# Optimization experiments

Hardware: AMD Instinct MI355X
Metric: run time of the kernel (lower is better)

The kernel has to match this reference:

```python
import jax, jax.numpy as jnp
import numpy as np

N_HEAD = 12
NEG_INF = -1e30


def setup_inputs() -> dict:
    key = jax.random.key(0)
    ks = jax.random.split(key, 12)
    bs, q_len, c_len, d = 2, 2048, 2048, 768
    s = 1.0 / np.sqrt(d)
    return {
        "query": jax.random.normal(ks[0], (bs, q_len, d), jnp.float32),
        "context": jax.random.normal(ks[1], (bs, c_len, d), jnp.float32),
        "c_mask": jax.random.randint(ks[2], (bs, c_len), 0, 2, jnp.int32),
        "Wq_w": jax.random.normal(ks[3], (d, d), jnp.float32) * s,
        "Wq_b": jnp.zeros((d,), jnp.float32),
        "Wk_w": jax.random.normal(ks[4], (d, d), jnp.float32) * s,
        "Wk_b": jnp.zeros((d,), jnp.float32),
        "Wv_w": jax.random.normal(ks[5], (d, d), jnp.float32) * s,
        "Wv_b": jnp.zeros((d,), jnp.float32),
        "fc_w": jax.random.normal(ks[6], (d, d), jnp.float32) * s,
        "fc_b": jnp.zeros((d,), jnp.float32),
    }


def reference(query, context, c_mask, Wq_w, Wq_b, Wk_w, Wk_b, Wv_w, Wv_b, fc_w, fc_b):
    bs, q_len, d = query.shape
    c_len = context.shape[1]
    d_k = d // N_HEAD
    a = 1.0 / np.sqrt(d_k)

    # QKV projections (torch Linear: y = x @ W.T + b), split into heads
    q = (query @ Wq_w.T + Wq_b).reshape(bs, q_len, N_HEAD, d_k)
    k = (context @ Wk_w.T + Wk_b).reshape(bs, c_len, N_HEAD, d_k)
    v = (context @ Wv_w.T + Wv_b).reshape(bs, c_len, N_HEAD, d_k)

    # scores [bs, n_head, q_len, c_len]
    s = jnp.einsum('bqhd,bchd->bhqc', q, k) * a

    # mask_logits: s * m + (1 - m) * -1e30, mask broadcast over heads and q
    m = c_mask.astype(s.dtype)[:, None, None, :]
    s = s * m + (1.0 - m) * NEG_INF

    p = jax.nn.softmax(s, axis=-1)  # dropout p=0.0 -> identity

    out = jnp.einsum('bhqc,bchd->bqhd', p, v).reshape(bs, q_len, d)
    return out @ fc_w.T + fc_b
```

## Files before the change

### kernel.cpp

```cpp
#include <hip/hip_runtime.h>
#include <cstdint>

#define D_MODEL 768
#define NH      12
#define DKH     64
#define SEQ     2048
#define BS      2
#define MROWS   (BS*SEQ)

typedef __bf16 bf16x8 __attribute__((ext_vector_type(8)));
typedef __bf16 bf16x4 __attribute__((ext_vector_type(4)));
typedef float  f32x4  __attribute__((ext_vector_type(4)));
typedef unsigned int u32_as1 __attribute__((address_space(1)));
typedef unsigned int u32_as3 __attribute__((address_space(3)));

__device__ __forceinline__ void gld16(const void* g, void* l) {
  __builtin_amdgcn_global_load_lds((const u32_as1*)g, (u32_as3*)l, 16, 0, 0);
}
__device__ __forceinline__ unsigned short f2bf(float x) {
  return __builtin_bit_cast(unsigned short, (__bf16)x);
}

__global__ void cvt_all(
    const float* __restrict__ q, const float* __restrict__ c,
    const float* __restrict__ wq, const float* __restrict__ wk,
    const float* __restrict__ wv, const float* __restrict__ wf,
    unsigned short* __restrict__ oq, unsigned short* __restrict__ oc,
    unsigned short* __restrict__ owq, unsigned short* __restrict__ owk,
    unsigned short* __restrict__ owv, unsigned short* __restrict__ owf)
{
  const int b = blockIdx.x;
  const float* in; unsigned short* out; int i;
  if (b < 6144) {
    in = (b < 3072) ? q : c;
    out = (b < 3072) ? oq : oc;
    i = ((b < 3072) ? b : b - 3072) * 256 + threadIdx.x;
  } else {
    int wb = b - 6144, wi = wb / 576;
    in  = (wi == 0) ? wq : (wi == 1) ? wk : (wi == 2) ? wv : wf;
    out = (wi == 0) ? owq : (wi == 1) ? owk : (wi == 2) ? owv : owf;
    i = (wb - wi * 576) * 256 + threadIdx.x;
  }
  float4 v = reinterpret_cast<const float4*>(in)[i];
  ushort4 o; o.x = f2bf(v.x); o.y = f2bf(v.y); o.z = f2bf(v.z); o.w = f2bf(v.w);
  reinterpret_cast<ushort4*>(out)[i] = o;
}

__global__ void mask_bf(const int* __restrict__ m, unsigned short* __restrict__ o) {
  int i = blockIdx.x * 256 + threadIdx.x;
  o[i] = f2bf(m[i] ? 1.0f : 0.0f);
}

template<bool OUT_F32>
__device__ __forceinline__ void gemm64x128_body(
    const unsigned short* __restrict__ A, const unsigned short* __restrict__ B,
    const float* __restrict__ bias, int biasRow, void* __restrict__ Cout,
    int ldc, int m0, int n0, float outScale, const int* __restrict__ colMask)
{
  __shared__ alignas(16) char sA[2][8192];
  __shared__ alignas(16) char sB[2][16384];
  const int tid = threadIdx.x;
  const int w = tid >> 6, l = tid & 63;
  const int g16 = l >> 4, c16 = l & 15;
  const int wr = (w >> 1) * 32, wc = (w & 1) * 64;

  auto stageA = [&](int kt, char* dst) {
#pragma unroll
    for (int i = 0; i < 2; i++) {
      int ch = w * 2 + i;
      int X = ch * 1024 + l * 16;
      int row = X >> 7;
      int sl = ((X >> 4) & 7) ^ (row & 7);
      gld16(A + (size_t)(m0 + row) * 768 + kt + sl * 8, dst + ch * 1024);
    }
  };
  auto stageB = [&](int kt, char* dst) {
#pragma unroll
    for (int i = 0; i < 4; i++) {
      int ch = w * 4 + i;
      int X = ch * 1024 + l * 16;
      int row = X >> 7;
      int sl = ((X >> 4) & 7) ^ (row & 7);
      gld16(B + (size_t)(n0 + row) * 768 + kt + sl * 8, dst + ch * 1024);
    }
  };

  f32x4 acc[2][4];
#pragma unroll
  for (int m = 0; m < 2; m++)
#pragma unroll
    for (int n = 0; n < 4; n++) acc[m][n] = f32x4{0.f, 0.f, 0.f, 0.f};

  stageA(0, sA[0]);
  stageB(0, sB[0]);
  __syncthreads();
  int cur = 0;
  for (int kt = 0; kt < 768; kt += 64) {
    if (kt + 64 < 768) {
      stageA(kt + 64, sA[cur ^ 1]);
      stageB(kt + 64, sB[cur ^ 1]);
    }
    __builtin_amdgcn_s_setprio(1);
#pragma unroll
    for (int kk = 0; kk < 2; kk++) {
      bf16x8 af[2], bq[4];
#pragma unroll
      for (int m = 0; m < 2; m++) {
        int row = wr + m * 16 + c16, slot = kk * 4 + g16;
        af[m] = *(const bf16x8*)(sA[cur] + row * 128 + ((slot ^ (row & 7)) << 4));
      }
#pragma unroll
      for (int n = 0; n < 4; n++) {
        int row = wc + n * 16 + c16, slot = kk * 4 + g16;
        bq[n] = *(const bf16x8*)(sB[cur] + row * 128 + ((slot ^ (row & 7)) << 4));
      }
#pragma unroll
      for (int m = 0; m < 2; m++)
#pragma unroll
        for (int n = 0; n < 4; n++)
          acc[m][n] = __builtin_amdgcn_mfma_f32_16x16x32_bf16(af[m], bq[n], acc[m][n], 0, 0, 0);
    }
    __builtin_amdgcn_s_setprio(0);
    __syncthreads();
    cur ^= 1;
  }

#pragma unroll
  for (int m = 0; m < 2; m++)
#pragma unroll
    for (int n = 0; n < 4; n++)
#pragma unroll
      for (int r = 0; r < 4; r++) {
        int row = m0 + wr + m * 16 + g16 * 4 + r;
        int col = n0 + wc + n * 16 + c16;
        float v = (acc[m][n][r] + (biasRow ? bias[row] : bias[col])) * outScale;
        if (colMask) v *= (float)colMask[col];
        if constexpr (OUT_F32) ((float*)Cout)[(size_t)row * ldc + col] = v;
        else ((unsigned short*)Cout)[(size_t)row * ldc + col] = f2bf(v);
      }
}

#define QSCALE 0.1803368801111f

__global__ __launch_bounds__(256, 2) void gemm_qkv(
    const unsigned short* __restrict__ q_bf, const unsigned short* __restrict__ c_bf,
    const unsigned short* __restrict__ wq, const unsigned short* __restrict__ wk,
    const unsigned short* __restrict__ wv,
    const float* __restrict__ bq, const float* __restrict__ bk,
    const float* __restrict__ bv, const int* __restrict__ cmask,
    unsigned short* __restrict__ Qb, unsigned short* __restrict__ Kb,
    unsigned short* __restrict__ Vtb)
{
  const int x = blockIdx.x;
  const int lin = (x & 7) * 48 + (x >> 3);
  if (blockIdx.y == 0) {
    gemm64x128_body<false>(q_bf, wq, bq, 0, Qb, 768, (lin / 6) * 64, (lin % 6) * 128,
                           QSCALE, nullptr);
  } else if (blockIdx.y == 1) {
    gemm64x128_body<false>(c_bf, wk, bk, 0, Kb, 768, (lin / 6) * 64, (lin % 6) * 128,
                           1.0f, nullptr);
  } else {
    gemm64x128_body<false>(wv, c_bf, bv, 1, Vtb, 4096, (lin % 12) * 64, (lin / 12) * 128,
                           1.0f, cmask);
  }
}

__global__ __launch_bounds__(256, 4) void gemm_fc64(
    const unsigned short* __restrict__ A, const unsigned short* __restrict__ B,
    const float* __restrict__ bias, float* __restrict__ Cout)
{
  __shared__ alignas(16) char sA[2][8192];
  __shared__ alignas(16) char sB[2][8192];
  const int tid = threadIdx.x;
  const int w = tid >> 6, l = tid & 63;
  const int g16 = l >> 4, c16 = l & 15;
  const int flat = blockIdx.x;
  const int lin = (flat & 7) * 96 + (flat >> 3);
  const int tf = lin % 12, ts = lin / 12;
  const int m0 = ts * 64, n0 = tf * 64;
  const int wr = (w >> 1) * 32, wc = (w & 1) * 32;

  auto stage = [&](const unsigned short* __restrict__ P, int p0, int kt, char* dst) {
#pragma unroll
    for (int i = 0; i < 2; i++) {
      int ch = w * 2 + i;
      int X = ch * 1024 + l * 16;
      int row = X >> 7;
      int sl = ((X >> 4) & 7) ^ (row & 7);
      gld16(P + (size_t)(p0 + row) * 768 + kt + sl * 8, dst + ch * 1024);
    }
  };

  f32x4 acc[2][2];
#pragma unroll
  for (int m = 0; m < 2; m++)
#pragma unroll
    for (int n = 0; n < 2; n++) acc[m][n] = f32x4{0.f, 0.f, 0.f, 0.f};

  stage(A, m0, 0, sA[0]);
  stage(B, n0, 0, sB[0]);
  __syncthreads();
  int cur = 0;
  for (int kt = 0; kt < 768; kt += 64) {
    if (kt + 64 < 768) {
      stage(A, m0, kt + 64, sA[cur ^ 1]);
      stage(B, n0, kt + 64, sB[cur ^ 1]);
    }
    __builtin_amdgcn_s_setprio(1);
#pragma unroll
    for (int kk = 0; kk < 2; kk++) {
      bf16x8 af[2], bq[2];
#pragma unroll
      for (int m = 0; m < 2; m++) {
        int row = wr + m * 16 + c16, slot = kk * 4 + g16;
        af[m] = *(const bf16x8*)(sA[cur] + row * 128 + ((slot ^ (row & 7)) << 4));
      }
#pragma unroll
      for (int n = 0; n < 2; n++) {
        int row = wc + n * 16 + c16, slot = kk * 4 + g16;
        bq[n] = *(const bf16x8*)(sB[cur] + row * 128 + ((slot ^ (row & 7)) << 4));
      }
#pragma unroll
      for (int m = 0; m < 2; m++)
#pragma unroll
        for (int n = 0; n < 2; n++)
          acc[m][n] = __builtin_amdgcn_mfma_f32_16x16x32_bf16(af[m], bq[n], acc[m][n], 0, 0, 0);
    }
    __builtin_amdgcn_s_setprio(0);
    __syncthreads();
    cur ^= 1;
  }

#pragma unroll
  for (int m = 0; m < 2; m++)
#pragma unroll
    for (int n = 0; n < 2; n++)
#pragma unroll
      for (int r = 0; r < 4; r++) {
        int row = m0 + wr + m * 16 + g16 * 4 + r;
        int col = n0 + wc + n * 16 + c16;
        Cout[(size_t)row * 768 + col] = acc[m][n][r] + bias[col];
      }
}

__global__ __launch_bounds__(256, 4) void attn_kernel(
    const unsigned short* __restrict__ Qb, const unsigned short* __restrict__ Kb,
    const unsigned short* __restrict__ Vt, const unsigned short* __restrict__ maskbf,
    unsigned short* __restrict__ Ob)
{
  __shared__ alignas(16) char sK[2][8192];
  __shared__ alignas(16) char sV[2][8192];
  const int tid = threadIdx.x, w = tid >> 6, l = tid & 63;
  const int g16 = l >> 4, c16 = l & 15;
  const int flat = blockIdx.x;
  const int xcd = flat & 7, sidx = flat >> 3;
  const int p = xcd + 8 * (sidx >> 5);
  const int qt = sidx & 31;
  const int h = p % 12, b = p / 12;
  const int qrow0 = b * SEQ + qt * 64;
  const int crow0 = b * SEQ;
  const int gLow = g16 >> 1, gOddB = (g16 & 1) * 8;

  bf16x8 qa[2];
  {
    const unsigned short* qp =
        Qb + (size_t)(qrow0 + w * 16 + c16) * D_MODEL + h * DKH + g16 * 8;
    qa[0] = *(const bf16x8*)(qp);
    qa[1] = *(const bf16x8*)(qp + 32);
  }

  auto stageK = [&](int ct, int buf) {
#pragma unroll
    for (int i = 0; i < 2; i++) {
      int ch = w * 2 + i;
      int X = ch * 1024 + l * 16;
      int row = X >> 7;
      int sl = ((X >> 4) & 7) ^ (row & 7);
      gld16(Kb + (size_t)(crow0 + ct + row) * D_MODEL + h * DKH + sl * 8,
            sK[buf] + ch * 1024);
    }
  };
  auto stageV = [&](int ct, int buf) {
#pragma unroll
    for (int i = 0; i < 2; i++) {
      int ch = w * 2 + i;
      int X = ch * 1024 + l * 16;
      int row = X >> 7;
      int sl = ((X >> 4) & 7) ^ (row & 7);
      gld16(Vt + (size_t)(h * DKH + row) * (size_t)MROWS + crow0 + ct + sl * 8,
            sV[buf] + ch * 1024);
    }
  };

  f32x4 accO[4], accL;
#pragma unroll
  for (int n = 0; n < 4; n++) accO[n] = f32x4{0.f, 0.f, 0.f, 0.f};
  accL = f32x4{0.f, 0.f, 0.f, 0.f};

  stageK(0, 0); stageV(0, 0);
  __syncthreads();
  int cur = 0;

  for (int ct = 0; ct < SEQ; ct += 64) {
    if (ct + 64 < SEQ) { stageK(ct + 64, cur ^ 1); stageV(ct + 64, cur ^ 1); }

    bf16x8 mfrag[2];
#pragma unroll
    for (int kk = 0; kk < 2; kk++) {
      const unsigned short* mp = maskbf + crow0 + ct + kk * 32 + g16 * 4;
      bf16x4 m0 = *(const bf16x4*)(mp);
      bf16x4 m1 = *(const bf16x4*)(mp + 16);
      mfrag[kk] = __builtin_shufflevector(m0, m1, 0, 1, 2, 3, 4, 5, 6, 7);
    }

    f32x4 s4[4];
#pragma unroll
    for (int n = 0; n < 4; n++) s4[n] = f32x4{0.f, 0.f, 0.f, 0.f};
    __builtin_amdgcn_s_setprio(1);
#pragma unroll
    for (int kk = 0; kk < 2; kk++) {
      bf16x8 kf[4];
#pragma unroll
      for (int n = 0; n < 4; n++) {
        int row = n * 16 + c16, slot = kk * 4 + g16;
        kf[n] = *(const bf16x8*)(sK[cur] + row * 128 + ((slot ^ (row & 7)) << 4));
      }
#pragma unroll
      for (int n = 0; n < 4; n++)
        s4[n] = __builtin_amdgcn_mfma_f32_16x16x32_bf16(kf[n], qa[kk], s4[n], 0, 0, 0);
    }
    __builtin_amdgcn_s_setprio(0);

    bf16x8 paf[2];
#pragma unroll
    for (int kk = 0; kk < 2; kk++)
#pragma unroll
      for (int j = 0; j < 4; j++) {
        paf[kk][j]     = (__bf16)__builtin_amdgcn_exp2f(s4[2 * kk][j]);
        paf[kk][j + 4] = (__bf16)__builtin_amdgcn_exp2f(s4[2 * kk + 1][j]);
      }

    __builtin_amdgcn_s_setprio(1);
#pragma unroll
    for (int kk = 0; kk < 2; kk++) {
#pragma unroll
      for (int n = 0; n < 4; n++) {
        int row = n * 16 + c16;
        const char* base = sV[cur] + row * 128 + gOddB;
        int s1 = kk * 4 + gLow, s2 = s1 + 2;
        bf16x4 v0 = *(const bf16x4*)(base + ((s1 ^ (row & 7)) << 4));
        bf16x4 v1 = *(const bf16x4*)(base + ((s2 ^ (row & 7)) << 4));
        bf16x8 vf = __builtin_shufflevector(v0, v1, 0, 1, 2, 3, 4, 5, 6, 7);
        accO[n] = __builtin_amdgcn_mfma_f32_16x16x32_bf16(paf[kk], vf, accO[n], 0, 0, 0);
      }
      accL = __builtin_amdgcn_mfma_f32_16x16x32_bf16(paf[kk], mfrag[kk], accL, 0, 0, 0);
    }
    __builtin_amdgcn_s_setprio(0);

    __syncthreads();
    cur ^= 1;
  }

#pragma unroll
  for (int r = 0; r < 4; r++) {
    float inv = 1.0f / accL[r];
#pragma unroll
    for (int n = 0; n < 4; n++) {
      int row = qrow0 + w * 16 + g16 * 4 + r;
      int col = h * DKH + n * 16 + c16;
      Ob[(size_t)row * D_MODEL + col] = f2bf(accO[n][r] * inv);
    }
  }
}

extern "C" void kernel_launch(void* const* d_in, const int* in_sizes, int n_in,
                              void* d_out, int out_size, void* d_ws, size_t ws_size,
                              hipStream_t stream) {
  const float* query   = (const float*)d_in[0];
  const float* context = (const float*)d_in[1];
  const int*   cmask   = (const int*)d_in[2];
  const float* Wq_w = (const float*)d_in[3];
  const float* Wq_b = (const float*)d_in[4];
  const float* Wk_w = (const float*)d_in[5];
  const float* Wk_b = (const float*)d_in[6];
  const float* Wv_w = (const float*)d_in[7];
  const float* Wv_b = (const float*)d_in[8];
  const float* fc_w = (const float*)d_in[9];
  const float* fc_b = (const float*)d_in[10];
  float* out = (float*)d_out;

  unsigned short* ws   = (unsigned short*)d_ws;
  const size_t NQ = (size_t)MROWS * D_MODEL;
  const size_t NW = (size_t)D_MODEL * D_MODEL;
  unsigned short* q_bf = ws;
  unsigned short* c_bf = q_bf + NQ;
  unsigned short* Qb   = c_bf + NQ;
  unsigned short* Kb   = Qb + NQ;
  unsigned short* Vtb  = Kb + NQ;
  unsigned short* Ob   = Vtb + NQ;
  unsigned short* wq   = Ob + NQ;
  unsigned short* wk   = wq + NW;
  unsigned short* wv   = wk + NW;
  unsigned short* wf   = wv + NW;
  unsigned short* maskbf = q_bf;

  cvt_all<<<8448, 256, 0, stream>>>(query, context, Wq_w, Wk_w, Wv_w, fc_w,
                                    q_bf, c_bf, wq, wk, wv, wf);

  gemm_qkv<<<dim3(384, 3), 256, 0, stream>>>(
      q_bf, c_bf, wq, wk, wv, Wq_b, Wk_b, Wv_b, cmask, Qb, Kb, Vtb);

  mask_bf<<<MROWS / 256, 256, 0, stream>>>(cmask, maskbf);

  attn_kernel<<<768, 256, 0, stream>>>(Qb, Kb, Vtb, maskbf, Ob);

  gemm_fc64<<<768, 256, 0, stream>>>(Ob, wf, fc_b, out);
}
```

Before: 94.08 us.

## Enlarge QKV GEMM tiles to 128x128 and fold mask conversion into cvt kernel

The QKV projection GEMM moves from 64x128 tiles to 128x128 tiles, so each wave computes a 64x64 sub-tile with a 4x4 MFMA accumulator array. This halves the grid and improves operand reuse, at the cost of more registers and LDS per block and fewer blocks available for latency hiding. Separately, the mask-to-bf16 conversion is merged into the cvt_all kernel as extra vectorized blocks, which removes one launch. The bf16 mask buffer now lives in the output buffer, since q_bf is no longer free at that point.

```diff
diff --git a/kernel.cpp b/kernel.cpp
--- a/kernel.cpp
+++ b/kernel.cpp
@@ -25,87 +25,83 @@
     const float* __restrict__ q, const float* __restrict__ c,
     const float* __restrict__ wq, const float* __restrict__ wk,
     const float* __restrict__ wv, const float* __restrict__ wf,
+    const int* __restrict__ m,
     unsigned short* __restrict__ oq, unsigned short* __restrict__ oc,
     unsigned short* __restrict__ owq, unsigned short* __restrict__ owk,
-    unsigned short* __restrict__ owv, unsigned short* __restrict__ owf)
+    unsigned short* __restrict__ owv, unsigned short* __restrict__ owf,
+    unsigned short* __restrict__ om)
 {
   const int b = blockIdx.x;
-  const float* in; unsigned short* out; int i;
-  if (b < 6144) {
-    in = (b < 3072) ? q : c;
-    out = (b < 3072) ? oq : oc;
-    i = ((b < 3072) ? b : b - 3072) * 256 + threadIdx.x;
+  if (b < 8448) {
+    const float* in; unsigned short* out; int i;
+    if (b < 6144) {
+      in = (b < 3072) ? q : c;
+      out = (b < 3072) ? oq : oc;
+      i = ((b < 3072) ? b : b - 3072) * 256 + threadIdx.x;
+    } else {
+      int wb = b - 6144, wi = wb / 576;
+      in  = (wi == 0) ? wq : (wi == 1) ? wk : (wi == 2) ? wv : wf;
+      out = (wi == 0) ? owq : (wi == 1) ? owk : (wi == 2) ? owv : owf;
+      i = (wb - wi * 576) * 256 + threadIdx.x;
+    }
+    float4 v = reinterpret_cast<const float4*>(in)[i];
+    ushort4 o; o.x = f2bf(v.x); o.y = f2bf(v.y); o.z = f2bf(v.z); o.w = f2bf(v.w);
+    reinterpret_cast<ushort4*>(out)[i] = o;
   } else {
-    int wb = b - 6144, wi = wb / 576;
-    in  = (wi == 0) ? wq : (wi == 1) ? wk : (wi == 2) ? wv : wf;
-    out = (wi == 0) ? owq : (wi == 1) ? owk : (wi == 2) ? owv : owf;
-    i = (wb - wi * 576) * 256 + threadIdx.x;
-  }
-  float4 v = reinterpret_cast<const float4*>(in)[i];
-  ushort4 o; o.x = f2bf(v.x); o.y = f2bf(v.y); o.z = f2bf(v.z); o.w = f2bf(v.w);
-  reinterpret_cast<ushort4*>(out)[i] = o;
-}
-
-__global__ void mask_bf(const int* __restrict__ m, unsigned short* __restrict__ o) {
-  int i = blockIdx.x * 256 + threadIdx.x;
-  o[i] = f2bf(m[i] ? 1.0f : 0.0f);
+    int i = (b - 8448) * 256 + threadIdx.x;
+    int4 mv = reinterpret_cast<const int4*>(m)[i];
+    ushort4 o;
+    o.x = f2bf(mv.x ? 1.f : 0.f); o.y = f2bf(mv.y ? 1.f : 0.f);
+    o.z = f2bf(mv.z ? 1.f : 0.f); o.w = f2bf(mv.w ? 1.f : 0.f);
+    reinterpret_cast<ushort4*>(om)[i] = o;
+  }
 }
 
 template<bool OUT_F32>
-__device__ __forceinline__ void gemm64x128_body(
+__device__ __forceinline__ void gemm128_body(
     const unsigned short* __restrict__ A, const unsigned short* __restrict__ B,
     const float* __restrict__ bias, int biasRow, void* __restrict__ Cout,
     int ldc, int m0, int n0, float outScale, const int* __restrict__ colMask)
 {
-  __shared__ alignas(16) char sA[2][8192];
+  __shared__ alignas(16) char sA[2][16384];
   __shared__ alignas(16) char sB[2][16384];
   const int tid = threadIdx.x;
   const int w = tid >> 6, l = tid & 63;
   const int g16 = l >> 4, c16 = l & 15;
-  const int wr = (w >> 1) * 32, wc = (w & 1) * 64;
-
-  auto stageA = [&](int kt, char* dst) {
-#pragma unroll
-    for (int i = 0; i < 2; i++) {
-      int ch = w * 2 + i;
-      int X = ch * 1024 + l * 16;
-      int row = X >> 7;
-      int sl = ((X >> 4) & 7) ^ (row & 7);
-      gld16(A + (size_t)(m0 + row) * 768 + kt + sl * 8, dst + ch * 1024);
-    }
-  };
-  auto stageB = [&](int kt, char* dst) {
+  const int wr = (w >> 1) * 64, wc = (w & 1) * 64;
+
+  auto stage = [&](const unsigned short* __restrict__ P, int p0, int kt, char* dst) {
 #pragma unroll
     for (int i = 0; i < 4; i++) {
       int ch = w * 4 + i;
       int X = ch * 1024 + l * 16;
       int row = X >> 7;
       int sl = ((X >> 4) & 7) ^ (row & 7);
-      gld16(B + (size_t)(n0 + row) * 768 + kt + sl * 8, dst + ch * 1024);
+      gld16(P + (size_t)(p0 + row) * 768 + kt + sl * 8, dst + ch * 1024);
     }
   };
 
-  f32x4 acc[2][4];
-#pragma unroll
-  for (int m = 0; m < 2; m++)
+  f32x4 acc[4][4];
+#pragma unroll
+  for (int m = 0; m < 4; m++)
 #pragma unroll
     for (int n = 0; n < 4; n++) acc[m][n] = f32x4{0.f, 0.f, 0.f, 0.f};
 
-  stageA(0, sA[0]);
-  stageB(0, sB[0]);
+  stage(A, m0, 0, sA[0]);
+  stage(B, n0, 0, sB[0]);
   __syncthreads();
   int cur = 0;
   for (int kt = 0; kt < 768; kt += 64) {
     if (kt + 64 < 768) {
-      stageA(kt + 64, sA[cur ^ 1]);
-      stageB(kt + 64, sB[cur ^ 1]);
+      stage(A, m0, kt + 64, sA[cur ^ 1]);
+      stage(B, n0, kt + 64, sB[cur ^ 1]);
     }
     __builtin_amdgcn_s_setprio(1);
 #pragma unroll
     for (int kk = 0; kk < 2; kk++) {
-      bf16x8 af[2], bq[4];
-#pragma unroll
-      for (int m = 0; m < 2; m++) {
+      bf16x8 af[4], bq[4];
+#pragma unroll
+      for (int m = 0; m < 4; m++) {
         int row = wr + m * 16 + c16, slot = kk * 4 + g16;
         af[m] = *(const bf16x8*)(sA[cur] + row * 128 + ((slot ^ (row & 7)) << 4));
       }
@@ -115,7 +111,7 @@
         bq[n] = *(const bf16x8*)(sB[cur] + row * 128 + ((slot ^ (row & 7)) << 4));
       }
 #pragma unroll
-      for (int m = 0; m < 2; m++)
+      for (int m = 0; m < 4; m++)
 #pragma unroll
         for (int n = 0; n < 4; n++)
           acc[m][n] = __builtin_amdgcn_mfma_f32_16x16x32_bf16(af[m], bq[n], acc[m][n], 0, 0, 0);
@@ -126,7 +122,7 @@
   }
 
 #pragma unroll
-  for (int m = 0; m < 2; m++)
+  for (int m = 0; m < 4; m++)
 #pragma unroll
     for (int n = 0; n < 4; n++)
 #pragma unroll
@@ -152,16 +148,16 @@
     unsigned short* __restrict__ Vtb)
 {
   const int x = blockIdx.x;
-  const int lin = (x & 7) * 48 + (x >> 3);
+  const int lin = (x & 7) * 24 + (x >> 3);
   if (blockIdx.y == 0) {
-    gemm64x128_body<false>(q_bf, wq, bq, 0, Qb, 768, (lin / 6) * 64, (lin % 6) * 128,
-                           QSCALE, nullptr);
+    gemm128_body<false>(q_bf, wq, bq, 0, Qb, 768, (lin / 6) * 128, (lin % 6) * 128,
+                        QSCALE, nullptr);
   } else if (blockIdx.y == 1) {
-    gemm64x128_body<false>(c_bf, wk, bk, 0, Kb, 768, (lin / 6) * 64, (lin % 6) * 128,
-                           1.0f, nullptr);
+    gemm128_body<false>(c_bf, wk, bk, 0, Kb, 768, (lin / 6) * 128, (lin % 6) * 128,
+                        1.0f, nullptr);
   } else {
-    gemm64x128_body<false>(wv, c_bf, bv, 1, Vtb, 4096, (lin % 12) * 64, (lin / 12) * 128,
-                           1.0f, cmask);
+    gemm128_body<false>(wv, c_bf, bv, 1, Vtb, 4096, (lin % 6) * 128, (lin / 6) * 128,
+                        1.0f, cmask);
   }
 }
 
@@ -402,16 +398,14 @@
   unsigned short* wk   = wq + NW;
   unsigned short* wv   = wk + NW;
   unsigned short* wf   = wv + NW;
-  unsigned short* maskbf = q_bf;
-
-  cvt_all<<<8448, 256, 0, stream>>>(query, context, Wq_w, Wk_w, Wv_w, fc_w,
-                                    q_bf, c_bf, wq, wk, wv, wf);
-
-  gemm_qkv<<<dim3(384, 3), 256, 0, stream>>>(
+  unsigned short* maskbf = (unsigned short*)d_out;
+
+  cvt_all<<<8452, 256, 0, stream>>>(query, context, Wq_w, Wk_w, Wv_w, fc_w, cmask,
+                                    q_bf, c_bf, wq, wk, wv, wf, maskbf);
+
+  gemm_qkv<<<dim3(192, 3), 256, 0, stream>>>(
       q_bf, c_bf, wq, wk, wv, Wq_b, Wk_b, Wv_b, cmask, Qb, Kb, Vtb);
 
-  mask_bf<<<MROWS / 256, 256, 0, stream>>>(cmask, maskbf);
-
   attn_kernel<<<768, 256, 0, stream>>>(Qb, Kb, Vtb, maskbf, Ob);
 
   gemm_fc64<<<768, 256, 0, stream>>>(Ob, wf, fc_b, out);
```

After: 99.33 us. 1.06x slower.
